# Kernel tuning notes

Measured on AMD Instinct MI355X. Metric: run time of the kernel, lower is better.

Reference implementation:

```python
import jax, jax.numpy as jnp
import numpy as np

# --- constants from DPINeuron.__init__ defaults ---
I0 = 5e-14
Ut = 0.025
kappa = (0.75 + 0.66) / 2
Cmem, Campa, Cshunt = 3e-12, 2e-12, 2e-12
Itau_mem = 1e-12; Igain_mem = 1e-12; Ith = 1e-12; Idc = 1e-12
refP = 0.0; Ipfb_th = 1e-12; Ipfb_norm = 1e-12
Itau_ampa = 1e-12; Igain_ampa = 1e-12
Itau_shunt = 1e-12; Igain_shunt = 1e-12
dt = 1e-3
tau_mem = Ut / kappa * Cmem / Itau_mem
tau_ampa = Ut / kappa * Campa / Itau_ampa
tau_shunt = Ut / kappa * Cshunt / Itau_shunt
alpha = Igain_mem / Itau_mem      # Igain_mem/Itau_mem parameter (non-trainable default)
beta = I0 / Itau_mem              # I0/Itau_mem parameter (non-trainable default)
SLOPE = 25.0                      # fast_sigmoid surrogate slope

# Round with straight-through estimator (identity backward)
@jax.custom_vjp
def ste_round(x):
    return jnp.round(x)
def _r_fwd(x):
    return jnp.round(x), None
def _r_bwd(_, g):
    return (g,)
ste_round.defvjp(_r_fwd, _r_bwd)

# fast_sigmoid surrogate spike: Heaviside forward, 1/(slope|x|+1)^2 backward
@jax.custom_vjp
def fast_sigmoid(x):
    return (x > 0).astype(x.dtype)
def _fs_fwd(x):
    return (x > 0).astype(x.dtype), x
def _fs_bwd(x, g):
    return (g / (SLOPE * jnp.abs(x) + 1.0) ** 2,)
fast_sigmoid.defvjp(_fs_fwd, _fs_bwd)

B, N_IN, N_OUT = 4096, 2048, 2048

def setup_inputs() -> dict:
    key = jax.random.key(0)
    k1, k2, k3 = jax.random.split(key, 3)
    X = jax.random.uniform(k1, (B, N_IN), dtype=jnp.float32)           # input spikes/activity
    # module inits W to 1.0; use small positive random fan-in counts for a nontrivial test
    W_ampa = jax.random.uniform(k2, (N_OUT, N_IN), dtype=jnp.float32) * 4.0
    W_shunt = jax.random.uniform(k3, (N_OUT, N_IN), dtype=jnp.float32) * 4.0
    Iw_ampa = jnp.float32(1e-12)
    Iw_shunt = jnp.float32(1e-12)
    Imem = jnp.full((B, N_OUT), I0, jnp.float32)
    Iampa = jnp.full((B, N_OUT), I0, jnp.float32)
    Ishunt = jnp.full((B, N_OUT), I0, jnp.float32)
    refractory = jnp.zeros((B, N_OUT), jnp.float32)
    return dict(X=X, W_ampa=W_ampa, W_shunt=W_shunt, Iw_ampa=Iw_ampa,
                Iw_shunt=Iw_shunt, Imem=Imem, Iampa=Iampa, Ishunt=Ishunt,
                refractory=refractory)

def reference(X, W_ampa, W_shunt, Iw_ampa, Iw_shunt, Imem, Iampa, Ishunt, refractory):
    Iahp = I0
    Inmda = I0
    # synaptic GEMMs with rounded (STE) weights: [B, n_in] @ [n_in, n_out]
    numSynAmpa = X @ ste_round(W_ampa).T
    numSynShunt = X @ ste_round(W_shunt).T

    dIampa = -Iampa / tau_ampa
    Iampa = Iampa + (Igain_ampa / Itau_ampa) * Iw_ampa * numSynAmpa
    dIshunt = -Ishunt / tau_shunt
    Ishunt = Ishunt + (Igain_shunt / Itau_shunt) * Iw_shunt * numSynShunt

    Iin = Idc + Iampa + Inmda - Ishunt
    Iin = Iin * (refractory <= 0).astype(Iin.dtype)
    Iin = jnp.maximum(Iin, I0)

    # positive feedback current
    Ifb = (I0 ** (1.0 / (kappa + 1.0))) * Imem ** (kappa / (kappa + 1.0)) \
          / (1.0 + jnp.exp(-Ipfb_norm * (Imem - Ipfb_th)))
    f_imem = Ifb / Itau_mem * (Imem + Igain_mem)

    dImem = (alpha * (Iin - Itau_mem - Iahp) - Imem
             - (Iahp / I0) * beta * Imem
             + jax.lax.stop_gradient(f_imem)) / (tau_mem * (1.0 + Igain_mem / Imem))
    Imem = jnp.maximum(Imem + dImem * dt, I0)
    Iampa = jnp.maximum(Iampa + dIampa * dt, I0)
    Ishunt = jnp.maximum(Ishunt + dIshunt * dt, I0)

    spike = fast_sigmoid(Imem - Ith)
    Imem = (1.0 - spike) * Imem + spike * I0
    refractory = jnp.maximum(refractory - dt, 0.0)
    refractory = (1.0 - spike) * refractory + spike * refP
    return spike, (Imem, Iampa, Ishunt, refractory)
```

## Files before the change

### kernel.cpp

```cpp
#include <hip/hip_runtime.h>
#include <cstdint>
#include <cstddef>

typedef __bf16 bf16x8 __attribute__((ext_vector_type(8)));
typedef float  f32x4  __attribute__((ext_vector_type(4)));

__device__ __forceinline__ unsigned short f2bf(float x) {
    unsigned int u = __builtin_bit_cast(unsigned int, x);
    u += 0x7fffu + ((u >> 16) & 1u);
    return (unsigned short)(u >> 16);
}

__global__ void convert_all(const float4* __restrict__ X,
                            const float4* __restrict__ Wa,
                            const float4* __restrict__ Ws,
                            ushort4* __restrict__ Xb,
                            ushort4* __restrict__ Wab,
                            ushort4* __restrict__ Wsb) {
    int i = blockIdx.x * 256 + threadIdx.x;
    if (i < 2097152) {
        float4 v = X[i];
        Xb[i] = make_ushort4(f2bf(v.x), f2bf(v.y), f2bf(v.z), f2bf(v.w));
    } else if (i < 3145728) {
        int t = i - 2097152;
        float4 v = Wa[t];
        Wab[t] = make_ushort4(f2bf(rintf(v.x)), f2bf(rintf(v.y)),
                              f2bf(rintf(v.z)), f2bf(rintf(v.w)));
    } else {
        int t = i - 3145728;
        float4 v = Ws[t];
        Wsb[t] = make_ushort4(f2bf(rintf(v.x)), f2bf(rintf(v.y)),
                              f2bf(rintf(v.z)), f2bf(rintf(v.w)));
    }
}


constexpr int NCOL     = 2048;
constexpr int ROWBYTES = NCOL * 2;

__device__ __forceinline__ void neuron_step(
    float nA, float nS, float Im, float Ia, float Is, float rf,
    float IwA, float IwS,
    float& o0, float& o1, float& o2, float& o3, float& o4)
{
    constexpr float I0f       = 5e-14f;
    constexpr float c_Itau    = 1e-12f;
    constexpr float c_Igain   = 1e-12f;
    constexpr float c_Idc     = 1e-12f;
    constexpr float c_Ith     = 1e-12f;
    constexpr float c_pfb_th  = 1e-12f;
    constexpr float c_pfb_nrm = 1e-12f;
    constexpr float c_dt      = 1e-3f;
    constexpr float c_beta    = 0.05f;
    const float c_tau_mem  = (float)(0.025 / 0.705 * 3.0);
    const float c_tau_syn  = (float)(0.025 / 0.705 * 2.0);
    const float c_p2       = (float)(0.705 / 1.705);
    const float c0         = __powf(I0f, (float)(1.0 / 1.705));

    float dIa = -Ia / c_tau_syn;
    float Ia1 = fmaf(IwA, nA, Ia);
    float dIs = -Is / c_tau_syn;
    float Is1 = fmaf(IwS, nS, Is);

    float Iin = c_Idc + Ia1 + I0f - Is1;
    Iin = (rf <= 0.0f) ? Iin : 0.0f;
    Iin = fmaxf(Iin, I0f);

    float sg  = 1.0f + __expf(-c_pfb_nrm * (Im - c_pfb_th));
    float Ifb = c0 * __powf(Im, c_p2) / sg;
    float fim = Ifb / c_Itau * (Im + c_Igain);

    float num = (Iin - c_Itau - I0f) - Im - c_beta * Im + fim;
    float den = c_tau_mem * (1.0f + c_Igain / Im);
    float Im1 = fmaxf(fmaf(num / den, c_dt, Im), I0f);
    float IaO = fmaxf(fmaf(dIa, c_dt, Ia1), I0f);
    float IsO = fmaxf(fmaf(dIs, c_dt, Is1), I0f);
    float spk = (Im1 - c_Ith > 0.0f) ? 1.0f : 0.0f;
    float ImO = (spk > 0.0f) ? I0f : Im1;
    float rf1 = fmaxf(rf - c_dt, 0.0f);
    float rfO = (spk > 0.0f) ? 0.0f : rf1;

    o0 = spk; o1 = ImO; o2 = IaO; o3 = IsO; o4 = rfO;
}

__global__ __launch_bounds__(256, 2) void dpi_fused(
    const unsigned short* __restrict__ Xb,
    const unsigned short* __restrict__ Wab,
    const unsigned short* __restrict__ Wsb,
    const float* __restrict__ pIwA, const float* __restrict__ pIwS,
    const float* __restrict__ Imem_in, const float* __restrict__ Iampa_in,
    const float* __restrict__ Ishunt_in, const float* __restrict__ refr_in,
    float* __restrict__ out)
{
    __shared__ __align__(16) char lds[68096];
    unsigned short* As  = (unsigned short*)lds;
    unsigned short* Bas = (unsigned short*)(lds + 16384);
    unsigned short* Bss = (unsigned short*)(lds + 32768);

    const int tid  = threadIdx.x;
    const int lane = tid & 63;
    const int wid  = tid >> 6;
    const int wr   = wid >> 1;
    const int wc   = wid & 1;
    const int bn   = blockIdx.x;
    const int bm   = blockIdx.y;

    int offq[4];
    const char* srcA[4]; const char* srcBa[4]; const char* srcBs[4];
#pragma unroll
    for (int q = 0; q < 4; ++q) {
        int off = (q * 4 + wid) * 1024 + lane * 16;
        int row = off >> 7;
        int cG  = ((off >> 4) & 7) ^ (row & 7);
        offq[q]  = off;
        srcA[q]  = (const char*)Xb  + (size_t)(bm * 128 + row) * ROWBYTES + cG * 16;
        srcBa[q] = (const char*)Wab + (size_t)(bn * 128 + row) * ROWBYTES + cG * 16;
        srcBs[q] = (const char*)Wsb + (size_t)(bn * 128 + row) * ROWBYTES + cG * 16;
    }

    int offA[2][4], offB[2][4];
#pragma unroll
    for (int kk = 0; kk < 2; ++kk) {
        int cs = ((kk * 4 + (lane >> 4)) ^ (lane & 7)) * 16;
#pragma unroll
        for (int m = 0; m < 4; ++m)
            offA[kk][m] = (wr * 64 + m * 16 + (lane & 15)) * 128 + cs;
#pragma unroll
        for (int n = 0; n < 4; ++n)
            offB[kk][n] = (wc * 64 + n * 16 + (lane & 15)) * 128 + cs;
    }

    f32x4 accA[4][4] = {};
    f32x4 accS[4][4] = {};

    const char* Ab  = (const char*)As;
    const char* Bab = (const char*)Bas;
    const char* Bsb = (const char*)Bss;

    for (int kt = 0; kt < 32; ++kt) {
        if (kt) __syncthreads();
#pragma unroll
        for (int q = 0; q < 4; ++q) {
            __builtin_amdgcn_global_load_lds(
                (__attribute__((address_space(1))) void*)(srcA[q] + kt * 128),
                (__attribute__((address_space(3))) void*)((char*)As + offq[q]), 16, 0, 0);
            __builtin_amdgcn_global_load_lds(
                (__attribute__((address_space(1))) void*)(srcBa[q] + kt * 128),
                (__attribute__((address_space(3))) void*)((char*)Bas + offq[q]), 16, 0, 0);
            __builtin_amdgcn_global_load_lds(
                (__attribute__((address_space(1))) void*)(srcBs[q] + kt * 128),
                (__attribute__((address_space(3))) void*)((char*)Bss + offq[q]), 16, 0, 0);
        }
        asm volatile("s_waitcnt vmcnt(0)" ::: "memory");
        __syncthreads();

#pragma unroll
        for (int kk = 0; kk < 2; ++kk) {
            bf16x8 a[4], ba[4], bs[4];
#pragma unroll
            for (int m = 0; m < 4; ++m)
                a[m]  = *(const bf16x8*)(Ab  + offA[kk][m]);
#pragma unroll
            for (int n = 0; n < 4; ++n) {
                ba[n] = *(const bf16x8*)(Bab + offB[kk][n]);
                bs[n] = *(const bf16x8*)(Bsb + offB[kk][n]);
            }
#pragma unroll
            for (int m = 0; m < 4; ++m) {
#pragma unroll
                for (int n = 0; n < 4; ++n) {
                    accA[m][n] = __builtin_amdgcn_mfma_f32_16x16x32_bf16(a[m], ba[n], accA[m][n], 0, 0, 0);
                    accS[m][n] = __builtin_amdgcn_mfma_f32_16x16x32_bf16(a[m], bs[n], accS[m][n], 0, 0, 0);
                }
            }
        }
    }

    const float IwA = pIwA[0];
    const float IwS = pIwS[0];

    float* ldsA = (float*)lds;
    float* ldsS = (float*)(lds + 34048);

    const float4* Im4 = (const float4*)Imem_in;
    const float4* Ia4 = (const float4*)Iampa_in;
    const float4* Is4 = (const float4*)Ishunt_in;
    const float4* Rf4 = (const float4*)refr_in;
    float4* o_spk = (float4*)out;
    float4* o_mem = (float4*)(out + (size_t)8388608);
    float4* o_amp = (float4*)(out + (size_t)16777216);
    float4* o_shn = (float4*)(out + (size_t)25165824);
    float4* o_ref = (float4*)(out + (size_t)33554432);

#pragma unroll
    for (int h = 0; h < 2; ++h) {
        __syncthreads();
        if (wr == h) {
#pragma unroll
            for (int m = 0; m < 4; ++m)
#pragma unroll
                for (int n = 0; n < 4; ++n)
#pragma unroll
                    for (int r = 0; r < 4; ++r) {
                        int R = m * 16 + (lane >> 4) * 4 + r;
                        int C = wc * 64 + n * 16 + (lane & 15);
                        ldsA[R * 133 + C] = accA[m][n][r];
                        ldsS[R * 133 + C] = accS[m][n][r];
                    }
        }
        __syncthreads();
#pragma unroll
        for (int k = 0; k < 8; ++k) {
            int f4  = tid + 256 * k;
            int r2  = f4 >> 5;
            int c4  = f4 & 31;
            float4 nA4 = *(const float4*)&ldsA[r2 * 133 + c4 * 4];
            float4 nS4 = *(const float4*)&ldsS[r2 * 133 + c4 * 4];
            int    B   = bm * 128 + h * 64 + r2;
            size_t g4  = (size_t)B * 512 + (size_t)bn * 32 + c4;

            float4 im = Im4[g4], ia = Ia4[g4], is = Is4[g4], rf = Rf4[g4];
            float4 spk, mem, amp, shn, ref;
            neuron_step(nA4.x, nS4.x, im.x, ia.x, is.x, rf.x, IwA, IwS,
                        spk.x, mem.x, amp.x, shn.x, ref.x);
            neuron_step(nA4.y, nS4.y, im.y, ia.y, is.y, rf.y, IwA, IwS,
                        spk.y, mem.y, amp.y, shn.y, ref.y);
            neuron_step(nA4.z, nS4.z, im.z, ia.z, is.z, rf.z, IwA, IwS,
                        spk.z, mem.z, amp.z, shn.z, ref.z);
            neuron_step(nA4.w, nS4.w, im.w, ia.w, is.w, rf.w, IwA, IwS,
                        spk.w, mem.w, amp.w, shn.w, ref.w);
            o_spk[g4] = spk;
            o_mem[g4] = mem;
            o_amp[g4] = amp;
            o_shn[g4] = shn;
            o_ref[g4] = ref;
        }
    }
}

extern "C" void kernel_launch(void* const* d_in, const int* in_sizes, int n_in,
                              void* d_out, int out_size, void* d_ws, size_t ws_size,
                              hipStream_t stream) {
    const float* X    = (const float*)d_in[0];
    const float* Wa   = (const float*)d_in[1];
    const float* Ws   = (const float*)d_in[2];
    const float* IwA  = (const float*)d_in[3];
    const float* IwS  = (const float*)d_in[4];
    const float* Imem = (const float*)d_in[5];
    const float* Iamp = (const float*)d_in[6];
    const float* Ishn = (const float*)d_in[7];
    const float* refr = (const float*)d_in[8];

    unsigned short* Xb  = (unsigned short*)d_ws;
    unsigned short* Wab = Xb + (size_t)4096 * 2048;
    unsigned short* Wsb = Wab + (size_t)2048 * 2048;

    convert_all<<<16384, 256, 0, stream>>>((const float4*)X, (const float4*)Wa,
                                           (const float4*)Ws, (ushort4*)Xb,
                                           (ushort4*)Wab, (ushort4*)Wsb);

    dim3 grid(16, 32);
    dpi_fused<<<grid, 256, 0, stream>>>(Xb, Wab, Wsb, IwA, IwS,
                                        Imem, Iamp, Ishn, refr, (float*)d_out);
}
```

Measured before the change: 145.3 us.

## Switch GEMM operands from bf16 to fp8 and use fp8 MFMA

The conversion kernel now quantizes X and the rounded weights to fp8 instead of bf16. The fused kernel uses fp8 16x16x32 MFMA with 8-byte fragments, halving the K-loop trip count and the bytes moved per tile. Rounded weights in 0..4 are exact in fp8, but X (uniform floats) loses precision, which risks accuracy and could change spike outcomes near the threshold.

```diff
diff --git a/kernel.cpp b/kernel.cpp
--- a/kernel.cpp
+++ b/kernel.cpp
@@ -2,41 +2,34 @@
 #include <cstdint>
 #include <cstddef>
 
-typedef __bf16 bf16x8 __attribute__((ext_vector_type(8)));
-typedef float  f32x4  __attribute__((ext_vector_type(4)));
-
-__device__ __forceinline__ unsigned short f2bf(float x) {
-    unsigned int u = __builtin_bit_cast(unsigned int, x);
-    u += 0x7fffu + ((u >> 16) & 1u);
-    return (unsigned short)(u >> 16);
-}
+typedef float f32x4 __attribute__((ext_vector_type(4)));
+typedef long long i64;
 
 __global__ void convert_all(const float4* __restrict__ X,
                             const float4* __restrict__ Wa,
                             const float4* __restrict__ Ws,
-                            ushort4* __restrict__ Xb,
-                            ushort4* __restrict__ Wab,
-                            ushort4* __restrict__ Wsb) {
+                            unsigned long long* __restrict__ Xq,
+                            unsigned long long* __restrict__ Waq,
+                            unsigned long long* __restrict__ Wsq) {
     int i = blockIdx.x * 256 + threadIdx.x;
-    if (i < 2097152) {
-        float4 v = X[i];
-        Xb[i] = make_ushort4(f2bf(v.x), f2bf(v.y), f2bf(v.z), f2bf(v.w));
-    } else if (i < 3145728) {
-        int t = i - 2097152;
-        float4 v = Wa[t];
-        Wab[t] = make_ushort4(f2bf(rintf(v.x)), f2bf(rintf(v.y)),
-                              f2bf(rintf(v.z)), f2bf(rintf(v.w)));
-    } else {
-        int t = i - 3145728;
-        float4 v = Ws[t];
-        Wsb[t] = make_ushort4(f2bf(rintf(v.x)), f2bf(rintf(v.y)),
-                              f2bf(rintf(v.z)), f2bf(rintf(v.w)));
-    }
-}
-
-
-constexpr int NCOL     = 2048;
-constexpr int ROWBYTES = NCOL * 2;
+    const float4* s; unsigned long long* d; int t; bool rnd;
+    if (i < 1048576)      { s = X;  d = Xq;  t = i;           rnd = false; }
+    else if (i < 1572864) { s = Wa; d = Waq; t = i - 1048576; rnd = true;  }
+    else                  { s = Ws; d = Wsq; t = i - 1572864; rnd = true;  }
+    float4 a = s[2 * t], b = s[2 * t + 1];
+    if (rnd) {
+        a.x = rintf(a.x); a.y = rintf(a.y); a.z = rintf(a.z); a.w = rintf(a.w);
+        b.x = rintf(b.x); b.y = rintf(b.y); b.z = rintf(b.z); b.w = rintf(b.w);
+    }
+    int w0 = __builtin_amdgcn_cvt_pk_fp8_f32(a.x, a.y, 0, false);
+    w0     = __builtin_amdgcn_cvt_pk_fp8_f32(a.z, a.w, w0, true);
+    int w1 = __builtin_amdgcn_cvt_pk_fp8_f32(b.x, b.y, 0, false);
+    w1     = __builtin_amdgcn_cvt_pk_fp8_f32(b.z, b.w, w1, true);
+    d[t] = ((unsigned long long)(unsigned int)w1 << 32) | (unsigned int)w0;
+}
+
+
+constexpr int SRCROW = 2048;
 
 __device__ __forceinline__ void neuron_step(
     float nA, float nS, float Im, float Ia, float Is, float rf,
@@ -84,18 +77,18 @@
 }
 
 __global__ __launch_bounds__(256, 2) void dpi_fused(
-    const unsigned short* __restrict__ Xb,
-    const unsigned short* __restrict__ Wab,
-    const unsigned short* __restrict__ Wsb,
+    const unsigned char* __restrict__ Xq,
+    const unsigned char* __restrict__ Waq,
+    const unsigned char* __restrict__ Wsq,
     const float* __restrict__ pIwA, const float* __restrict__ pIwS,
     const float* __restrict__ Imem_in, const float* __restrict__ Iampa_in,
     const float* __restrict__ Ishunt_in, const float* __restrict__ refr_in,
     float* __restrict__ out)
 {
     __shared__ __align__(16) char lds[68096];
-    unsigned short* As  = (unsigned short*)lds;
-    unsigned short* Bas = (unsigned short*)(lds + 16384);
-    unsigned short* Bss = (unsigned short*)(lds + 32768);
+    char* As  = lds;
+    char* Bas = lds + 16384;
+    char* Bss = lds + 32768;
 
     const int tid  = threadIdx.x;
     const int lane = tid & 63;
@@ -106,71 +99,71 @@
     const int bm   = blockIdx.y;
 
     int offq[4];
-    const char* srcA[4]; const char* srcBa[4]; const char* srcBs[4];
+    const unsigned char* srcA[4];
+    const unsigned char* srcBa[4];
+    const unsigned char* srcBs[4];
 #pragma unroll
     for (int q = 0; q < 4; ++q) {
         int off = (q * 4 + wid) * 1024 + lane * 16;
         int row = off >> 7;
         int cG  = ((off >> 4) & 7) ^ (row & 7);
         offq[q]  = off;
-        srcA[q]  = (const char*)Xb  + (size_t)(bm * 128 + row) * ROWBYTES + cG * 16;
-        srcBa[q] = (const char*)Wab + (size_t)(bn * 128 + row) * ROWBYTES + cG * 16;
-        srcBs[q] = (const char*)Wsb + (size_t)(bn * 128 + row) * ROWBYTES + cG * 16;
-    }
-
-    int offA[2][4], offB[2][4];
-#pragma unroll
-    for (int kk = 0; kk < 2; ++kk) {
-        int cs = ((kk * 4 + (lane >> 4)) ^ (lane & 7)) * 16;
-#pragma unroll
-        for (int m = 0; m < 4; ++m)
-            offA[kk][m] = (wr * 64 + m * 16 + (lane & 15)) * 128 + cs;
-#pragma unroll
-        for (int n = 0; n < 4; ++n)
-            offB[kk][n] = (wc * 64 + n * 16 + (lane & 15)) * 128 + cs;
-    }
+        srcA[q]  = Xq  + (size_t)(bm * 128 + row) * SRCROW + cG * 16;
+        srcBa[q] = Waq + (size_t)(bn * 128 + row) * SRCROW + cG * 16;
+        srcBs[q] = Wsq + (size_t)(bn * 128 + row) * SRCROW + cG * 16;
+    }
+
+    const int fr = lane & 15;
+    const int g  = lane >> 4;
+    int subk[4];
+#pragma unroll
+    for (int kk = 0; kk < 4; ++kk)
+        subk[kk] = ((((kk * 2) + (g >> 1)) ^ (fr & 7)) << 4) + (g & 1) * 8;
+    int rowA[4], rowB[4];
+#pragma unroll
+    for (int m = 0; m < 4; ++m)
+        rowA[m] = (wr * 64 + m * 16 + fr) * 128;
+#pragma unroll
+    for (int n = 0; n < 4; ++n)
+        rowB[n] = (wc * 64 + n * 16 + fr) * 128;
 
     f32x4 accA[4][4] = {};
     f32x4 accS[4][4] = {};
 
-    const char* Ab  = (const char*)As;
-    const char* Bab = (const char*)Bas;
-    const char* Bsb = (const char*)Bss;
-
-    for (int kt = 0; kt < 32; ++kt) {
+    for (int kt = 0; kt < 16; ++kt) {
         if (kt) __syncthreads();
 #pragma unroll
         for (int q = 0; q < 4; ++q) {
             __builtin_amdgcn_global_load_lds(
                 (__attribute__((address_space(1))) void*)(srcA[q] + kt * 128),
-                (__attribute__((address_space(3))) void*)((char*)As + offq[q]), 16, 0, 0);
+                (__attribute__((address_space(3))) void*)(As + offq[q]), 16, 0, 0);
             __builtin_amdgcn_global_load_lds(
                 (__attribute__((address_space(1))) void*)(srcBa[q] + kt * 128),
-                (__attribute__((address_space(3))) void*)((char*)Bas + offq[q]), 16, 0, 0);
+                (__attribute__((address_space(3))) void*)(Bas + offq[q]), 16, 0, 0);
             __builtin_amdgcn_global_load_lds(
                 (__attribute__((address_space(1))) void*)(srcBs[q] + kt * 128),
-                (__attribute__((address_space(3))) void*)((char*)Bss + offq[q]), 16, 0, 0);
+                (__attribute__((address_space(3))) void*)(Bss + offq[q]), 16, 0, 0);
         }
         asm volatile("s_waitcnt vmcnt(0)" ::: "memory");
         __syncthreads();
 
 #pragma unroll
-        for (int kk = 0; kk < 2; ++kk) {
-            bf16x8 a[4], ba[4], bs[4];
+        for (int kk = 0; kk < 4; ++kk) {
+            i64 a[4], ba[4], bs[4];
 #pragma unroll
             for (int m = 0; m < 4; ++m)
-                a[m]  = *(const bf16x8*)(Ab  + offA[kk][m]);
+                a[m]  = *(const i64*)(As  + rowA[m] + subk[kk]);
 #pragma unroll
             for (int n = 0; n < 4; ++n) {
-                ba[n] = *(const bf16x8*)(Bab + offB[kk][n]);
-                bs[n] = *(const bf16x8*)(Bsb + offB[kk][n]);
+                ba[n] = *(const i64*)(Bas + rowB[n] + subk[kk]);
+                bs[n] = *(const i64*)(Bss + rowB[n] + subk[kk]);
             }
 #pragma unroll
             for (int m = 0; m < 4; ++m) {
 #pragma unroll
                 for (int n = 0; n < 4; ++n) {
-                    accA[m][n] = __builtin_amdgcn_mfma_f32_16x16x32_bf16(a[m], ba[n], accA[m][n], 0, 0, 0);
-                    accS[m][n] = __builtin_amdgcn_mfma_f32_16x16x32_bf16(a[m], bs[n], accS[m][n], 0, 0, 0);
+                    accA[m][n] = __builtin_amdgcn_mfma_f32_16x16x32_fp8_fp8(a[m], ba[n], accA[m][n], 0, 0, 0);
+                    accS[m][n] = __builtin_amdgcn_mfma_f32_16x16x32_fp8_fp8(a[m], bs[n], accS[m][n], 0, 0, 0);
                 }
             }
         }
@@ -251,15 +244,17 @@
     const float* Ishn = (const float*)d_in[7];
     const float* refr = (const float*)d_in[8];
 
-    unsigned short* Xb  = (unsigned short*)d_ws;
-    unsigned short* Wab = Xb + (size_t)4096 * 2048;
-    unsigned short* Wsb = Wab + (size_t)2048 * 2048;
-
-    convert_all<<<16384, 256, 0, stream>>>((const float4*)X, (const float4*)Wa,
-                                           (const float4*)Ws, (ushort4*)Xb,
-                                           (ushort4*)Wab, (ushort4*)Wsb);
+    unsigned char* Xq  = (unsigned char*)d_ws;
+    unsigned char* Waq = Xq + (size_t)4096 * 2048;
+    unsigned char* Wsq = Waq + (size_t)2048 * 2048;
+
+    convert_all<<<8192, 256, 0, stream>>>((const float4*)X, (const float4*)Wa,
+                                          (const float4*)Ws,
+                                          (unsigned long long*)Xq,
+                                          (unsigned long long*)Waq,
+                                          (unsigned long long*)Wsq);
 
     dim3 grid(16, 32);
-    dpi_fused<<<grid, 256, 0, stream>>>(Xb, Wab, Wsb, IwA, IwS,
+    dpi_fused<<<grid, 256, 0, stream>>>(Xq, Waq, Wsq, IwA, IwS,
                                         Imem, Iamp, Ishn, refr, (float*)d_out);
 }
```

Result: faster. 139.9 us (-3.7%).
